# Performance work log

Measured on AMD Instinct MI355X. Metric: run time of the kernel, lower is better.

## Reference

```python
import jax, jax.numpy as jnp
import numpy as np

CUTOFF = 0.32178
SCALE = 2.0 * 28.0 * CUTOFF


def setup_inputs() -> dict:
    rng = np.random.default_rng(0)
    N, E0, K = 20000, 160000, 9
    pos_np = rng.uniform(0.0, 28.0, (N, 2)).astype(np.float32)
    s = rng.integers(0, N, E0)
    d = rng.integers(0, N, E0)
    keep = s != d
    ei = np.stack([s[keep], d[keep]])
    ei = np.concatenate([ei, ei[::-1]], axis=1)
    ei = np.unique(ei.T, axis=0).T.astype(np.int64)  # symmetric, deduped, no self-loops

    def ncut(ei_, pos_):
        r, c = ei_
        w = np.linalg.norm(pos_[r] - pos_[c], axis=1)
        deg = np.bincount(r, minlength=pos_.shape[0]).astype(np.float64)
        deg[deg == 0] = 1.0
        return w * (1.0 / deg[r] + 1.0 / deg[c])

    def graclus(ei_, w, n):
        # greedy heavy-weight matching in node-index order (graclus-style)
        o = np.argsort(ei_[0], kind='stable')
        r, c, ww = ei_[0][o], ei_[1][o], w[o]
        ptr = np.searchsorted(r, np.arange(n + 1))
        cl = -np.ones(n, dtype=np.int64)
        cid = 0
        for i in range(n):
            if cl[i] >= 0:
                continue
            best, bw = -1, -1.0
            for k in range(ptr[i], ptr[i + 1]):
                j = c[k]
                if cl[j] < 0 and j != i and ww[k] > bw:
                    bw, best = ww[k], j
            cl[i] = cid
            if best >= 0:
                cl[best] = cid
            cid += 1
        return cl, cid

    def pool_edges(ei_, cl):
        m = cl[ei_]
        m = m[:, m[0] != m[1]]
        return np.unique(m.T, axis=0).T

    def seg_mean(v, cl, c):
        out = np.zeros((c, v.shape[1]), dtype=np.float64)
        np.add.at(out, cl, v)
        cnt = np.bincount(cl, minlength=c).astype(np.float64)
        return (out / cnt[:, None]).astype(np.float32)

    cl1, C1 = graclus(ei, ncut(ei, pos_np), N)
    ei2 = pool_edges(ei, cl1)
    pos2 = seg_mean(pos_np, cl1, C1)
    cl2, C2 = graclus(ei2, ncut(ei2, pos2), C1)
    ei3 = pool_edges(ei2, cl2)

    def prm(*shape):
        return jnp.asarray(rng.normal(0.0, 0.1, shape).astype(np.float32))

    def sig(k):
        return jnp.asarray(rng.uniform(0.5, 1.5, (k, 2)).astype(np.float32))

    return {
        'x': jnp.asarray(rng.standard_normal((N, 1)).astype(np.float32)),
        'pos': jnp.asarray(pos_np),
        'edge_index1': jnp.asarray(ei, dtype=jnp.int32),
        'cluster1': jnp.asarray(cl1, dtype=jnp.int32),
        'edge_index2': jnp.asarray(ei2, dtype=jnp.int32),
        'cluster2': jnp.asarray(cl2, dtype=jnp.int32),
        'edge_index3': jnp.asarray(ei3, dtype=jnp.int32),
        'batch': jnp.zeros((C2,), dtype=jnp.int32),
        'g1': prm(1, K, 32), 'mu1': prm(K, 2) + 0.5, 'sigma1': sig(K), 'root1': prm(1, 32), 'b1': prm(32),
        'g2': prm(32, K, 64), 'mu2': prm(K, 2) + 0.5, 'sigma2': sig(K), 'root2': prm(32, 64), 'b2': prm(64),
        'g3': prm(64, K, 64), 'mu3': prm(K, 2) + 0.5, 'sigma3': sig(K), 'root3': prm(64, 64), 'b3': prm(64),
        'fw': prm(64, 128), 'fb': prm(128),
    }


def _pseudo(pos, ei):
    # edge pseudo-coordinates: (pos[col]-pos[row]) / (2*28*cutoff) + 0.5
    return (pos[ei[1]] - pos[ei[0]]) / SCALE + 0.5


def _gmm_conv(x, ei, ea, g, mu, sigma, root, bias, n):
    # GMMConv: mean over neighbors of sum_k gauss_k(e_ij) * (x_j @ G_k), plus root weight and bias
    row, col = ei[0], ei[1]
    d = ea[:, None, :] - mu[None]                                       # [E,K,2]
    w = jnp.exp(-0.5 * jnp.sum(d * d / (sigma[None] ** 2), axis=-1))    # [E,K]
    msg = jnp.einsum('ei,iko,ek->eo', x[row], g, w)                     # [E,out]
    agg = jax.ops.segment_sum(msg, col, num_segments=n)
    cnt = jax.ops.segment_sum(jnp.ones_like(col, dtype=x.dtype), col, num_segments=n)
    return agg / jnp.maximum(cnt, 1.0)[:, None] + x @ root + bias


def _seg_mean(v, seg, n):
    s = jax.ops.segment_sum(v, seg, num_segments=n)
    c = jax.ops.segment_sum(jnp.ones((v.shape[0],), v.dtype), seg, num_segments=n)
    return s / jnp.maximum(c, 1.0)[:, None]


def _forward(x, pos, edge_index1, cluster1, edge_index2, cluster2, edge_index3, batch,
             g1, mu1, sigma1, root1, b1, g2, mu2, sigma2, root2, b2,
             g3, mu3, sigma3, root3, b3, fw, fb):
    N = x.shape[0]
    C1 = cluster2.shape[0]
    C2 = batch.shape[0]
    h = jax.nn.elu(_gmm_conv(x, edge_index1, _pseudo(pos, edge_index1), g1, mu1, sigma1, root1, b1, N))
    h = jax.ops.segment_max(h, cluster1, num_segments=C1)               # max_pool x
    pos2 = _seg_mean(pos, cluster1, C1)                                  # max_pool pos (mean)
    h = jax.nn.elu(_gmm_conv(h, edge_index2, _pseudo(pos2, edge_index2), g2, mu2, sigma2, root2, b2, C1))
    h = jax.ops.segment_max(h, cluster2, num_segments=C2)
    pos3 = _seg_mean(pos2, cluster2, C2)
    h = jax.nn.elu(_gmm_conv(h, edge_index3, _pseudo(pos3, edge_index3), g3, mu3, sigma3, root3, b3, C2))
    gm = _seg_mean(h, batch, 1)                                          # global_mean_pool (1 graph)
    return gm @ fw + fb                                                  # forward returns fc1(x)


def reference(x, pos, edge_index1, cluster1, edge_index2, cluster2, edge_index3, batch,
              g1, mu1, sigma1, root1, b1, g2, mu2, sigma2, root2, b2,
              g3, mu3, sigma3, root3, b3, fw, fb):
    return _forward(x, pos, edge_index1, cluster1, edge_index2, cluster2, edge_index3, batch,
                    g1, mu1, sigma1, root1, b1, g2, mu2, sigma2, root2, b2,
                    g3, mu3, sigma3, root3, b3, fw, fb)
```

## Files before the change

### kernel.cpp

```cpp
#include <hip/hip_runtime.h>
#include <math.h>

static constexpr float SCALE_F = (float)(2.0 * 28.0 * 0.32178);

__device__ __forceinline__ unsigned mapf(float f){
    unsigned u = __float_as_uint(f);
    return (u & 0x80000000u) ? ~u : (u | 0x80000000u);
}
__device__ __forceinline__ float unmapf(unsigned m){
    unsigned u = (m & 0x80000000u) ? (m ^ 0x80000000u) : ~m;
    return __uint_as_float(u);
}
__device__ __forceinline__ float eluf(float x){ return x > 0.f ? x : expm1f(x); }

__device__ __forceinline__ void wave_sync(){
    __builtin_amdgcn_wave_barrier();
    asm volatile("s_waitcnt lgkmcnt(0)" ::: "memory");
    __builtin_amdgcn_wave_barrier();
}

__global__ void prep_kernel(const float* __restrict__ x, const float* __restrict__ pos, int N,
    const int* __restrict__ ei1, int E1, const int* __restrict__ ei2, int E2, int C1,
    const int* __restrict__ ei3, int E3, int C2,
    int* __restrict__ rp1, int* __restrict__ rp2, int* __restrict__ rp3,
    unsigned* __restrict__ hmax, int nmax, float* __restrict__ zreg, int nz,
    float4* __restrict__ xp1)
{
    int i0 = blockIdx.x*blockDim.x + threadIdx.x, gs = gridDim.x*blockDim.x;
    for (int i = i0; i < nmax; i += gs) hmax[i] = 0x007FFFFFu;
    for (int i = i0; i < nz;   i += gs) zreg[i] = 0.f;
    for (int i = i0; i < N;    i += gs) xp1[i] = make_float4(pos[2*i], pos[2*i+1], x[i], 0.f);
    int nrp = N + C1 + C2 + 3;
    for (int i = i0; i < nrp; i += gs){
        const int* rows; int E, n; int* rp;
        if (i <= N)            { rows = ei1; E = E1; n = i;            rp = rp1 + n; }
        else if (i <= N+1+C1)  { rows = ei2; E = E2; n = i - (N+1);    rp = rp2 + n; }
        else                   { rows = ei3; E = E3; n = i - (N+C1+2); rp = rp3 + n; }
        int lo = 0, hi = E;
        while (lo < hi){ int m = (lo+hi) >> 1; if (rows[m] < n) lo = m+1; else hi = m; }
        *rp = lo;
    }
}

__global__ __launch_bounds__(256) void l1_kernel(const float4* __restrict__ xp1,
    const int* __restrict__ ei1, int E1, const int* __restrict__ rp1, const int* __restrict__ cl1,
    const float* __restrict__ g1, const float* __restrict__ mu1, const float* __restrict__ sg1,
    const float* __restrict__ rt1, const float* __restrict__ b1,
    unsigned* __restrict__ h2m, float4* __restrict__ pos2s4, int N)
{
    int t = threadIdx.x;
    int lane = t & 63, wv = t >> 6;
    int q = lane >> 4, il = lane & 15;
    int n = (blockIdx.x*4 + wv)*4 + q;
    if (n >= N) return;
    const int* cols = ei1 + E1;
    float mx[9], my[9], ivx[9], ivy[9];
    #pragma unroll
    for (int k = 0; k < 9; k++){
        mx[k] = mu1[2*k]; my[k] = mu1[2*k+1];
        float sx = sg1[2*k], sy = sg1[2*k+1];
        ivx[k] = 1.f/(sx*sx); ivy[k] = 1.f/(sy*sy);
    }
    float4 me = xp1[n];
    float px = me.x, py = me.y, xn = me.z;
    int e0 = rp1[n], e1 = rp1[n+1];
    float s[9] = {0.f,0.f,0.f,0.f,0.f,0.f,0.f,0.f,0.f};
    for (int e = e0 + il; e < e1; e += 16){
        int j = cols[e];
        float4 pj = xp1[j];
        float ux = (px - pj.x)/SCALE_F + 0.5f;
        float uy = (py - pj.y)/SCALE_F + 0.5f;
        #pragma unroll
        for (int k = 0; k < 9; k++){
            float dx = ux - mx[k], dy = uy - my[k];
            s[k] += pj.z * expf(-0.5f*(dx*dx*ivx[k] + dy*dy*ivy[k]));
        }
    }
    #pragma unroll
    for (int off = 8; off > 0; off >>= 1){
        #pragma unroll
        for (int k = 0; k < 9; k++) s[k] += __shfl_xor(s[k], off, 16);
    }
    float inv = 1.f / (float)max(e1 - e0, 1);
    int c = cl1[n];
    #pragma unroll
    for (int oo = 0; oo < 2; oo++){
        int o = il + oo*16;
        float acc = 0.f;
        #pragma unroll
        for (int k = 0; k < 9; k++) acc += g1[k*32+o] * s[k];
        float v = acc*inv + xn*rt1[o] + b1[o];
        atomicMax(&h2m[(size_t)c*32 + o], mapf(eluf(v)));
    }
    if (il == 0){
        atomicAdd(&pos2s4[c].x, px);
        atomicAdd(&pos2s4[c].y, py);
        atomicAdd(&pos2s4[c].z, 1.f);
    }
}

__global__ __launch_bounds__(256) void l2_kernel(const unsigned* __restrict__ h2m,
    const float4* __restrict__ pos2s4,
    const int* __restrict__ ei2, int E2, const int* __restrict__ rp2, const int* __restrict__ cl2,
    const float* __restrict__ g2, const float* __restrict__ mu2, const float* __restrict__ sg2,
    const float* __restrict__ rt2, const float* __restrict__ b2,
    unsigned* __restrict__ h3m, float4* __restrict__ pos3s4, int C1)
{
    __shared__ float wbuf[4][576];
    __shared__ int   jcs[4][64];
    __shared__ float xns[4][32];
    int t = threadIdx.x, l = t & 63, w = t >> 6;
    int n = blockIdx.x*4 + w;
    if (n >= C1) return;
    const int* cols = ei2 + E2;
    float mx[9], my[9], ivx[9], ivy[9];
    #pragma unroll
    for (int k = 0; k < 9; k++){
        mx[k] = mu2[2*k]; my[k] = mu2[2*k+1];
        float sx = sg2[2*k], sy = sg2[2*k+1];
        ivx[k] = 1.f/(sx*sx); ivy[k] = 1.f/(sy*sy);
    }
    if (l < 32) xns[w][l] = unmapf(h2m[(size_t)n*32 + l]);
    float4 pm = pos2s4[n];
    float cn = fmaxf(pm.z, 1.f);
    float px = pm.x/cn, py = pm.y/cn;
    int e0 = rp2[n], e1 = rp2[n+1], deg = e1 - e0;
    int i = l & 31, half = l >> 5;
    float sacc[9] = {0.f,0.f,0.f,0.f,0.f,0.f,0.f,0.f,0.f};
    for (int base = e0; base < e1; base += 64){
        int ne = min(64, e1 - base);
        if (l < ne){
            int j = cols[base + l];
            jcs[w][l] = j;
            float4 pj = pos2s4[j];
            float cj = fmaxf(pj.z, 1.f);
            float ux = (px - pj.x/cj)/SCALE_F + 0.5f;
            float uy = (py - pj.y/cj)/SCALE_F + 0.5f;
            #pragma unroll
            for (int k = 0; k < 9; k++){
                float dx = ux - mx[k], dy = uy - my[k];
                wbuf[w][l*9+k] = expf(-0.5f*(dx*dx*ivx[k] + dy*dy*ivy[k]));
            }
        }
        wave_sync();
        for (int jj = half; jj < ne; jj += 2){
            int j = jcs[w][jj];
            float xji = unmapf(h2m[(size_t)j*32 + i]);
            #pragma unroll
            for (int k = 0; k < 9; k++) sacc[k] += xji * wbuf[w][jj*9+k];
        }
        wave_sync();
    }
    #pragma unroll
    for (int k = 0; k < 9; k++) sacc[k] += __shfl_xor(sacc[k], 32, 64);
    if (l < 32){
        #pragma unroll
        for (int k = 0; k < 9; k++) wbuf[w][l*9+k] = sacc[k];
    }
    wave_sync();
    float acc = 0.f;
    #pragma unroll 8
    for (int idx = 0; idx < 288; idx++) acc += g2[idx*64 + l] * wbuf[w][idx];
    float racc = 0.f;
    #pragma unroll 8
    for (int ii = 0; ii < 32; ii++) racc += xns[w][ii] * rt2[ii*64 + l];
    float inv = 1.f / (float)max(deg, 1);
    float h = eluf(acc*inv + racc + b2[l]);
    int c = cl2[n];
    atomicMax(&h3m[(size_t)c*64 + l], mapf(h));
    if (l == 0){
        atomicAdd(&pos3s4[c].x, px);
        atomicAdd(&pos3s4[c].y, py);
        atomicAdd(&pos3s4[c].z, 1.f);
    }
}

__global__ __launch_bounds__(256) void l3_kernel(const unsigned* __restrict__ h3m,
    const float4* __restrict__ pos3s4,
    const int* __restrict__ ei3, int E3, const int* __restrict__ rp3,
    const float* __restrict__ g3, const float* __restrict__ mu3, const float* __restrict__ sg3,
    const float* __restrict__ rt3, const float* __restrict__ b3,
    float* __restrict__ gpart, int C2)
{
    __shared__ float wbuf[4][576];
    __shared__ int   jcs[4][64];
    __shared__ float xns[4][64];
    int t = threadIdx.x, l = t & 63, w = t >> 6;
    int n = blockIdx.x*4 + w;
    if (n >= C2) return;
    const int* cols = ei3 + E3;
    float mx[9], my[9], ivx[9], ivy[9];
    #pragma unroll
    for (int k = 0; k < 9; k++){
        mx[k] = mu3[2*k]; my[k] = mu3[2*k+1];
        float sx = sg3[2*k], sy = sg3[2*k+1];
        ivx[k] = 1.f/(sx*sx); ivy[k] = 1.f/(sy*sy);
    }
    xns[w][l] = unmapf(h3m[(size_t)n*64 + l]);
    float4 pm = pos3s4[n];
    float cn = fmaxf(pm.z, 1.f);
    float px = pm.x/cn, py = pm.y/cn;
    int e0 = rp3[n], e1 = rp3[n+1], deg = e1 - e0;
    float sacc[9] = {0.f,0.f,0.f,0.f,0.f,0.f,0.f,0.f,0.f};
    for (int base = e0; base < e1; base += 64){
        int ne = min(64, e1 - base);
        if (l < ne){
            int j = cols[base + l];
            jcs[w][l] = j;
            float4 pj = pos3s4[j];
            float cj = fmaxf(pj.z, 1.f);
            float ux = (px - pj.x/cj)/SCALE_F + 0.5f;
            float uy = (py - pj.y/cj)/SCALE_F + 0.5f;
            #pragma unroll
            for (int k = 0; k < 9; k++){
                float dx = ux - mx[k], dy = uy - my[k];
                wbuf[w][l*9+k] = expf(-0.5f*(dx*dx*ivx[k] + dy*dy*ivy[k]));
            }
        }
        wave_sync();
        for (int jj = 0; jj < ne; jj++){
            int j = jcs[w][jj];
            float xji = unmapf(h3m[(size_t)j*64 + l]);
            #pragma unroll
            for (int k = 0; k < 9; k++) sacc[k] += xji * wbuf[w][jj*9+k];
        }
        wave_sync();
    }
    #pragma unroll
    for (int k = 0; k < 9; k++) wbuf[w][l*9+k] = sacc[k];
    wave_sync();
    float acc = 0.f;
    #pragma unroll 8
    for (int idx = 0; idx < 576; idx++) acc += g3[idx*64 + l] * wbuf[w][idx];
    float racc = 0.f;
    #pragma unroll 8
    for (int ii = 0; ii < 64; ii++) racc += xns[w][ii] * rt3[ii*64 + l];
    float inv = 1.f / (float)max(deg, 1);
    float h = eluf(acc*inv + racc + b3[l]);
    atomicAdd(&gpart[(size_t)(n & 63)*64 + l], h);
}

__global__ void final_kernel(const float* __restrict__ gpart, const float* __restrict__ fw,
                             const float* __restrict__ fb, float* __restrict__ out, int C2){
    __shared__ float gs[64];
    __shared__ float red[2*64];
    int t = threadIdx.x;
    int o = t & 63, h = t >> 6;
    float a = 0.f;
    for (int p = h*32; p < h*32 + 32; p++) a += gpart[p*64 + o];
    red[h*64 + o] = a;
    __syncthreads();
    if (t < 64) gs[t] = (red[t] + red[64+t]) / (float)C2;
    __syncthreads();
    float acc = fb[t];
    for (int o2 = 0; o2 < 64; o2++) acc += gs[o2] * fw[o2*128 + t];
    out[t] = acc;
}

extern "C" void kernel_launch(void* const* d_in, const int* in_sizes, int n_in,
                              void* d_out, int out_size, void* d_ws, size_t ws_size,
                              hipStream_t stream)
{
    const float* x    = (const float*)d_in[0];
    const float* pos  = (const float*)d_in[1];
    const int*   ei1  = (const int*)d_in[2];
    const int*   cl1  = (const int*)d_in[3];
    const int*   ei2  = (const int*)d_in[4];
    const int*   cl2  = (const int*)d_in[5];
    const int*   ei3  = (const int*)d_in[6];
    const float* g1   = (const float*)d_in[8];
    const float* mu1  = (const float*)d_in[9];
    const float* sg1  = (const float*)d_in[10];
    const float* rt1  = (const float*)d_in[11];
    const float* b1   = (const float*)d_in[12];
    const float* g2   = (const float*)d_in[13];
    const float* mu2  = (const float*)d_in[14];
    const float* sg2  = (const float*)d_in[15];
    const float* rt2  = (const float*)d_in[16];
    const float* b2   = (const float*)d_in[17];
    const float* g3   = (const float*)d_in[18];
    const float* mu3  = (const float*)d_in[19];
    const float* sg3  = (const float*)d_in[20];
    const float* rt3  = (const float*)d_in[21];
    const float* b3   = (const float*)d_in[22];
    const float* fw   = (const float*)d_in[23];
    const float* fb   = (const float*)d_in[24];
    float* out = (float*)d_out;

    const int N  = in_sizes[0];
    const int E1 = in_sizes[2] / 2;
    const int C1 = in_sizes[5];
    const int E2 = in_sizes[4] / 2;
    const int C2 = in_sizes[7];
    const int E3 = in_sizes[6] / 2;

    float* w = (float*)d_ws;
    size_t off = 0;
    float4* xp1    = (float4*)(w + off); off += (size_t)4*N;
    float4* pos2s4 = (float4*)(w + off); off += (size_t)4*C1;
    float4* pos3s4 = (float4*)(w + off); off += (size_t)4*C2;
    float*  gpart  = w + off;            off += 64*64;
    int* rp1 = (int*)(w + off); off += (size_t)N + 1;
    int* rp2 = (int*)(w + off); off += (size_t)C1 + 1;
    int* rp3 = (int*)(w + off); off += (size_t)C2 + 1;
    unsigned* h2m = (unsigned*)(w + off); off += (size_t)C1 * 32;
    unsigned* h3m = (unsigned*)(w + off); off += (size_t)C2 * 64;

    const int nmax = C1*32 + C2*64;
    const int nz   = 4*C1 + 4*C2 + 64*64;
    prep_kernel<<<dim3(1024), dim3(256), 0, stream>>>(x, pos, N,
        ei1, E1, ei2, E2, C1, ei3, E3, C2,
        rp1, rp2, rp3, h2m, nmax, (float*)pos2s4, nz, xp1);

    l1_kernel<<<dim3((N + 15)/16), dim3(256), 0, stream>>>(xp1, ei1, E1, rp1, cl1,
        g1, mu1, sg1, rt1, b1, h2m, pos2s4, N);
    l2_kernel<<<dim3((C1 + 3)/4), dim3(256), 0, stream>>>(h2m, pos2s4, ei2, E2, rp2, cl2,
        g2, mu2, sg2, rt2, b2, h3m, pos3s4, C1);
    l3_kernel<<<dim3((C2 + 3)/4), dim3(256), 0, stream>>>(h3m, pos3s4, ei3, E3, rp3,
        g3, mu3, sg3, rt3, b3, gpart, C2);
    final_kernel<<<dim3(1), dim3(128), 0, stream>>>(gpart, fw, fb, out, C2);
}
```

Baseline: 229.2 us.

## Replace atomic max/mean pooling with pair-gather pooling and split conv layers

Pooling no longer uses atomicMax into order-mapped integers or atomicAdd for centroids. A prep pass instead records the min and max node index of each cluster, and new pool kernels take the elementwise max and mean of those two members. Layers 2 and 3 are each split into an aggregation kernel, which writes per-node 9xC sums to a workspace buffer, and a dense projection kernel. Both use float4 LDS layouts and unrolled gather loops. This relies on every cluster having at most two members, which graclus matching guarantees. It adds several kernel launches and extra global round-trips for the intermediate sums.

```diff
diff --git a/kernel.cpp b/kernel.cpp
--- a/kernel.cpp
+++ b/kernel.cpp
@@ -3,14 +3,6 @@
 
 static constexpr float SCALE_F = (float)(2.0 * 28.0 * 0.32178);
 
-__device__ __forceinline__ unsigned mapf(float f){
-    unsigned u = __float_as_uint(f);
-    return (u & 0x80000000u) ? ~u : (u | 0x80000000u);
-}
-__device__ __forceinline__ float unmapf(unsigned m){
-    unsigned u = (m & 0x80000000u) ? (m ^ 0x80000000u) : ~m;
-    return __uint_as_float(u);
-}
 __device__ __forceinline__ float eluf(float x){ return x > 0.f ? x : expm1f(x); }
 
 __device__ __forceinline__ void wave_sync(){
@@ -19,17 +11,33 @@
     __builtin_amdgcn_wave_barrier();
 }
 
+__global__ void initk(int* __restrict__ mlo1, int* __restrict__ mhi1, int C1,
+                      int* __restrict__ mlo2, int* __restrict__ mhi2, int C2,
+                      float* __restrict__ gpart){
+    int i = blockIdx.x*blockDim.x + threadIdx.x, gs = gridDim.x*blockDim.x;
+    for (int c = i; c < C1; c += gs){ mlo1[c] = 0x7FFFFFFF; mhi1[c] = -1; }
+    for (int c = i; c < C2; c += gs){ mlo2[c] = 0x7FFFFFFF; mhi2[c] = -1; }
+    for (int k = i; k < 64*64; k += gs) gpart[k] = 0.f;
+}
+
 __global__ void prep_kernel(const float* __restrict__ x, const float* __restrict__ pos, int N,
     const int* __restrict__ ei1, int E1, const int* __restrict__ ei2, int E2, int C1,
     const int* __restrict__ ei3, int E3, int C2,
+    const int* __restrict__ cl1, const int* __restrict__ cl2,
     int* __restrict__ rp1, int* __restrict__ rp2, int* __restrict__ rp3,
-    unsigned* __restrict__ hmax, int nmax, float* __restrict__ zreg, int nz,
+    int* __restrict__ mlo1, int* __restrict__ mhi1, int* __restrict__ mlo2, int* __restrict__ mhi2,
     float4* __restrict__ xp1)
 {
     int i0 = blockIdx.x*blockDim.x + threadIdx.x, gs = gridDim.x*blockDim.x;
-    for (int i = i0; i < nmax; i += gs) hmax[i] = 0x007FFFFFu;
-    for (int i = i0; i < nz;   i += gs) zreg[i] = 0.f;
-    for (int i = i0; i < N;    i += gs) xp1[i] = make_float4(pos[2*i], pos[2*i+1], x[i], 0.f);
+    for (int i = i0; i < N; i += gs){
+        xp1[i] = make_float4(pos[2*i], pos[2*i+1], x[i], 0.f);
+        int c = cl1[i];
+        atomicMin(&mlo1[c], i); atomicMax(&mhi1[c], i);
+    }
+    for (int i = i0; i < C1; i += gs){
+        int c = cl2[i];
+        atomicMin(&mlo2[c], i); atomicMax(&mhi2[c], i);
+    }
     int nrp = N + C1 + C2 + 3;
     for (int i = i0; i < nrp; i += gs){
         const int* rows; int E, n; int* rp;
@@ -43,10 +51,10 @@
 }
 
 __global__ __launch_bounds__(256) void l1_kernel(const float4* __restrict__ xp1,
-    const int* __restrict__ ei1, int E1, const int* __restrict__ rp1, const int* __restrict__ cl1,
+    const int* __restrict__ ei1, int E1, const int* __restrict__ rp1,
     const float* __restrict__ g1, const float* __restrict__ mu1, const float* __restrict__ sg1,
     const float* __restrict__ rt1, const float* __restrict__ b1,
-    unsigned* __restrict__ h2m, float4* __restrict__ pos2s4, int N)
+    float* __restrict__ h1, int N)
 {
     int t = threadIdx.x;
     int lane = t & 63, wv = t >> 6;
@@ -82,33 +90,43 @@
         for (int k = 0; k < 9; k++) s[k] += __shfl_xor(s[k], off, 16);
     }
     float inv = 1.f / (float)max(e1 - e0, 1);
-    int c = cl1[n];
     #pragma unroll
     for (int oo = 0; oo < 2; oo++){
         int o = il + oo*16;
         float acc = 0.f;
         #pragma unroll
         for (int k = 0; k < 9; k++) acc += g1[k*32+o] * s[k];
-        float v = acc*inv + xn*rt1[o] + b1[o];
-        atomicMax(&h2m[(size_t)c*32 + o], mapf(eluf(v)));
-    }
-    if (il == 0){
-        atomicAdd(&pos2s4[c].x, px);
-        atomicAdd(&pos2s4[c].y, py);
-        atomicAdd(&pos2s4[c].z, 1.f);
-    }
-}
-
-__global__ __launch_bounds__(256) void l2_kernel(const unsigned* __restrict__ h2m,
+        h1[(size_t)n*32 + o] = eluf(acc*inv + xn*rt1[o] + b1[o]);
+    }
+}
+
+__global__ void pool1_kernel(const float* __restrict__ h1, const float4* __restrict__ xp1,
+    const int* __restrict__ mlo1, const int* __restrict__ mhi1,
+    float* __restrict__ h2, float4* __restrict__ pos2s4, int C1)
+{
+    int i0 = blockIdx.x*blockDim.x + threadIdx.x, gs = gridDim.x*blockDim.x;
+    for (int idx = i0; idx < C1*32; idx += gs){
+        int c = idx >> 5, i = idx & 31;
+        h2[idx] = fmaxf(h1[(size_t)mlo1[c]*32 + i], h1[(size_t)mhi1[c]*32 + i]);
+    }
+    for (int c = i0; c < C1; c += gs){
+        int a = mlo1[c], b = mhi1[c];
+        float4 pa = xp1[a];
+        float px, py;
+        if (a == b){ px = pa.x; py = pa.y; }
+        else { float4 pb = xp1[b]; px = (pa.x + pb.x)/2.f; py = (pa.y + pb.y)/2.f; }
+        pos2s4[c] = make_float4(px, py, 0.f, 0.f);
+    }
+}
+
+__global__ __launch_bounds__(256) void l2a_kernel(const float* __restrict__ h2,
     const float4* __restrict__ pos2s4,
-    const int* __restrict__ ei2, int E2, const int* __restrict__ rp2, const int* __restrict__ cl2,
-    const float* __restrict__ g2, const float* __restrict__ mu2, const float* __restrict__ sg2,
-    const float* __restrict__ rt2, const float* __restrict__ b2,
-    unsigned* __restrict__ h3m, float4* __restrict__ pos3s4, int C1)
-{
-    __shared__ float wbuf[4][576];
-    __shared__ int   jcs[4][64];
-    __shared__ float xns[4][32];
+    const int* __restrict__ ei2, int E2, const int* __restrict__ rp2,
+    const float* __restrict__ mu2, const float* __restrict__ sg2,
+    float* __restrict__ S2, int C1)
+{
+    __shared__ __align__(16) float wbuf[4][768];
+    __shared__ int jcs[4][64];
     int t = threadIdx.x, l = t & 63, w = t >> 6;
     int n = blockIdx.x*4 + w;
     if (n >= C1) return;
@@ -120,11 +138,9 @@
         float sx = sg2[2*k], sy = sg2[2*k+1];
         ivx[k] = 1.f/(sx*sx); ivy[k] = 1.f/(sy*sy);
     }
-    if (l < 32) xns[w][l] = unmapf(h2m[(size_t)n*32 + l]);
     float4 pm = pos2s4[n];
-    float cn = fmaxf(pm.z, 1.f);
-    float px = pm.x/cn, py = pm.y/cn;
-    int e0 = rp2[n], e1 = rp2[n+1], deg = e1 - e0;
+    float px = pm.x, py = pm.y;
+    int e0 = rp2[n], e1 = rp2[n+1];
     int i = l & 31, half = l >> 5;
     float sacc[9] = {0.f,0.f,0.f,0.f,0.f,0.f,0.f,0.f,0.f};
     for (int base = e0; base < e1; base += 64){
@@ -133,21 +149,48 @@
             int j = cols[base + l];
             jcs[w][l] = j;
             float4 pj = pos2s4[j];
-            float cj = fmaxf(pj.z, 1.f);
-            float ux = (px - pj.x/cj)/SCALE_F + 0.5f;
-            float uy = (py - pj.y/cj)/SCALE_F + 0.5f;
+            float ux = (px - pj.x)/SCALE_F + 0.5f;
+            float uy = (py - pj.y)/SCALE_F + 0.5f;
+            float wk[9];
             #pragma unroll
             for (int k = 0; k < 9; k++){
                 float dx = ux - mx[k], dy = uy - my[k];
-                wbuf[w][l*9+k] = expf(-0.5f*(dx*dx*ivx[k] + dy*dy*ivy[k]));
+                wk[k] = expf(-0.5f*(dx*dx*ivx[k] + dy*dy*ivy[k]));
             }
+            *(float4*)&wbuf[w][l*12]     = make_float4(wk[0], wk[1], wk[2], wk[3]);
+            *(float4*)&wbuf[w][l*12 + 4] = make_float4(wk[4], wk[5], wk[6], wk[7]);
+            wbuf[w][l*12 + 8] = wk[8];
         }
         wave_sync();
-        for (int jj = half; jj < ne; jj += 2){
+        int jj = half;
+        for (; jj + 6 < ne; jj += 8){
+            int j0 = jcs[w][jj],   j1 = jcs[w][jj+2];
+            int j2 = jcs[w][jj+4], j3 = jcs[w][jj+6];
+            float x0 = h2[(size_t)j0*32 + i];
+            float x1 = h2[(size_t)j1*32 + i];
+            float x2 = h2[(size_t)j2*32 + i];
+            float x3 = h2[(size_t)j3*32 + i];
+            #pragma unroll
+            for (int u = 0; u < 4; u++){
+                int jc = jj + 2*u;
+                float xv = (u==0)?x0:(u==1)?x1:(u==2)?x2:x3;
+                float4 wa = *(const float4*)&wbuf[w][jc*12];
+                float4 wb = *(const float4*)&wbuf[w][jc*12 + 4];
+                float  w8 = wbuf[w][jc*12 + 8];
+                sacc[0] += xv*wa.x; sacc[1] += xv*wa.y; sacc[2] += xv*wa.z; sacc[3] += xv*wa.w;
+                sacc[4] += xv*wb.x; sacc[5] += xv*wb.y; sacc[6] += xv*wb.z; sacc[7] += xv*wb.w;
+                sacc[8] += xv*w8;
+            }
+        }
+        for (; jj < ne; jj += 2){
             int j = jcs[w][jj];
-            float xji = unmapf(h2m[(size_t)j*32 + i]);
-            #pragma unroll
-            for (int k = 0; k < 9; k++) sacc[k] += xji * wbuf[w][jj*9+k];
+            float xv = h2[(size_t)j*32 + i];
+            float4 wa = *(const float4*)&wbuf[w][jj*12];
+            float4 wb = *(const float4*)&wbuf[w][jj*12 + 4];
+            float  w8 = wbuf[w][jj*12 + 8];
+            sacc[0] += xv*wa.x; sacc[1] += xv*wa.y; sacc[2] += xv*wa.z; sacc[3] += xv*wa.w;
+            sacc[4] += xv*wb.x; sacc[5] += xv*wb.y; sacc[6] += xv*wb.z; sacc[7] += xv*wb.w;
+            sacc[8] += xv*w8;
         }
         wave_sync();
     }
@@ -155,36 +198,83 @@
     for (int k = 0; k < 9; k++) sacc[k] += __shfl_xor(sacc[k], 32, 64);
     if (l < 32){
         #pragma unroll
-        for (int k = 0; k < 9; k++) wbuf[w][l*9+k] = sacc[k];
-    }
+        for (int k = 0; k < 9; k++) S2[(size_t)n*288 + l*9 + k] = sacc[k];
+    }
+}
+
+__global__ __launch_bounds__(256) void l2b_kernel(const float* __restrict__ S2,
+    const float* __restrict__ h2, const int* __restrict__ rp2,
+    const float* __restrict__ g2, const float* __restrict__ rt2, const float* __restrict__ b2,
+    float* __restrict__ h2out, int C1)
+{
+    __shared__ __align__(16) float sbuf[4][288];
+    __shared__ __align__(16) float xns[4][32];
+    int t = threadIdx.x, l = t & 63, w = t >> 6;
+    int n = blockIdx.x*4 + w;
+    if (n >= C1) return;
+    const float4* srow = (const float4*)(S2 + (size_t)n*288);
+    *(float4*)&sbuf[w][l*4] = srow[l];
+    if (l < 8) *(float4*)&sbuf[w][(64+l)*4] = srow[64+l];
+    if (l < 32) xns[w][l] = h2[(size_t)n*32 + l];
     wave_sync();
+    const float* gcol = g2 + l;
     float acc = 0.f;
-    #pragma unroll 8
-    for (int idx = 0; idx < 288; idx++) acc += g2[idx*64 + l] * wbuf[w][idx];
+    #pragma unroll 4
+    for (int qq = 0; qq < 36; qq++){
+        int ib = qq*8;
+        float g0 = gcol[(ib+0)*64], g1v = gcol[(ib+1)*64];
+        float g2v = gcol[(ib+2)*64], g3 = gcol[(ib+3)*64];
+        float g4 = gcol[(ib+4)*64], g5 = gcol[(ib+5)*64];
+        float g6 = gcol[(ib+6)*64], g7 = gcol[(ib+7)*64];
+        float4 sa = *(const float4*)&sbuf[w][ib];
+        float4 sb = *(const float4*)&sbuf[w][ib+4];
+        acc += g0*sa.x; acc += g1v*sa.y; acc += g2v*sa.z; acc += g3*sa.w;
+        acc += g4*sb.x; acc += g5*sb.y; acc += g6*sb.z; acc += g7*sb.w;
+    }
+    const float* rcol = rt2 + l;
     float racc = 0.f;
-    #pragma unroll 8
-    for (int ii = 0; ii < 32; ii++) racc += xns[w][ii] * rt2[ii*64 + l];
+    #pragma unroll 2
+    for (int qq = 0; qq < 4; qq++){
+        int ib = qq*8;
+        float4 xa = *(const float4*)&xns[w][ib];
+        float4 xb = *(const float4*)&xns[w][ib+4];
+        racc += rcol[(ib+0)*64]*xa.x; racc += rcol[(ib+1)*64]*xa.y;
+        racc += rcol[(ib+2)*64]*xa.z; racc += rcol[(ib+3)*64]*xa.w;
+        racc += rcol[(ib+4)*64]*xb.x; racc += rcol[(ib+5)*64]*xb.y;
+        racc += rcol[(ib+6)*64]*xb.z; racc += rcol[(ib+7)*64]*xb.w;
+    }
+    int deg = rp2[n+1] - rp2[n];
     float inv = 1.f / (float)max(deg, 1);
-    float h = eluf(acc*inv + racc + b2[l]);
-    int c = cl2[n];
-    atomicMax(&h3m[(size_t)c*64 + l], mapf(h));
-    if (l == 0){
-        atomicAdd(&pos3s4[c].x, px);
-        atomicAdd(&pos3s4[c].y, py);
-        atomicAdd(&pos3s4[c].z, 1.f);
-    }
-}
-
-__global__ __launch_bounds__(256) void l3_kernel(const unsigned* __restrict__ h3m,
+    h2out[(size_t)n*64 + l] = eluf(acc*inv + racc + b2[l]);
+}
+
+__global__ void pool2_kernel(const float* __restrict__ h2out, const float4* __restrict__ pos2s4,
+    const int* __restrict__ mlo2, const int* __restrict__ mhi2,
+    float* __restrict__ h3, float4* __restrict__ pos3s4, int C2)
+{
+    int i0 = blockIdx.x*blockDim.x + threadIdx.x, gs = gridDim.x*blockDim.x;
+    for (int idx = i0; idx < C2*64; idx += gs){
+        int c = idx >> 6, i = idx & 63;
+        h3[idx] = fmaxf(h2out[(size_t)mlo2[c]*64 + i], h2out[(size_t)mhi2[c]*64 + i]);
+    }
+    for (int c = i0; c < C2; c += gs){
+        int a = mlo2[c], b = mhi2[c];
+        float4 pa = pos2s4[a];
+        float px, py;
+        if (a == b){ px = pa.x; py = pa.y; }
+        else { float4 pb = pos2s4[b]; px = (pa.x + pb.x)/2.f; py = (pa.y + pb.y)/2.f; }
+        pos3s4[c] = make_float4(px, py, 0.f, 0.f);
+    }
+}
+
+__global__ __launch_bounds__(256) void l3a_kernel(const float* __restrict__ h3,
     const float4* __restrict__ pos3s4,
     const int* __restrict__ ei3, int E3, const int* __restrict__ rp3,
-    const float* __restrict__ g3, const float* __restrict__ mu3, const float* __restrict__ sg3,
-    const float* __restrict__ rt3, const float* __restrict__ b3,
-    float* __restrict__ gpart, int C2)
-{
-    __shared__ float wbuf[4][576];
-    __shared__ int   jcs[4][64];
-    __shared__ float xns[4][64];
+    const float* __restrict__ mu3, const float* __restrict__ sg3,
+    float* __restrict__ S3, int C2)
+{
+    __shared__ __align__(16) float wbuf[4][768];
+    __shared__ int jcs[4][64];
     int t = threadIdx.x, l = t & 63, w = t >> 6;
     int n = blockIdx.x*4 + w;
     if (n >= C2) return;
@@ -196,11 +286,9 @@
         float sx = sg3[2*k], sy = sg3[2*k+1];
         ivx[k] = 1.f/(sx*sx); ivy[k] = 1.f/(sy*sy);
     }
-    xns[w][l] = unmapf(h3m[(size_t)n*64 + l]);
     float4 pm = pos3s4[n];
-    float cn = fmaxf(pm.z, 1.f);
-    float px = pm.x/cn, py = pm.y/cn;
-    int e0 = rp3[n], e1 = rp3[n+1], deg = e1 - e0;
+    float px = pm.x, py = pm.y;
+    int e0 = rp3[n], e1 = rp3[n+1];
     float sacc[9] = {0.f,0.f,0.f,0.f,0.f,0.f,0.f,0.f,0.f};
     for (int base = e0; base < e1; base += 64){
         int ne = min(64, e1 - base);
@@ -208,33 +296,98 @@
             int j = cols[base + l];
             jcs[w][l] = j;
             float4 pj = pos3s4[j];
-            float cj = fmaxf(pj.z, 1.f);
-            float ux = (px - pj.x/cj)/SCALE_F + 0.5f;
-            float uy = (py - pj.y/cj)/SCALE_F + 0.5f;
+            float ux = (px - pj.x)/SCALE_F + 0.5f;
+            float uy = (py - pj.y)/SCALE_F + 0.5f;
+            float wk[9];
             #pragma unroll
             for (int k = 0; k < 9; k++){
                 float dx = ux - mx[k], dy = uy - my[k];
-                wbuf[w][l*9+k] = expf(-0.5f*(dx*dx*ivx[k] + dy*dy*ivy[k]));
+                wk[k] = expf(-0.5f*(dx*dx*ivx[k] + dy*dy*ivy[k]));
             }
+            *(float4*)&wbuf[w][l*12]     = make_float4(wk[0], wk[1], wk[2], wk[3]);
+            *(float4*)&wbuf[w][l*12 + 4] = make_float4(wk[4], wk[5], wk[6], wk[7]);
+            wbuf[w][l*12 + 8] = wk[8];
         }
         wave_sync();
-        for (int jj = 0; jj < ne; jj++){
+        int jj = 0;
+        for (; jj + 3 < ne; jj += 4){
+            int j0 = jcs[w][jj],   j1 = jcs[w][jj+1];
+            int j2 = jcs[w][jj+2], j3 = jcs[w][jj+3];
+            float x0 = h3[(size_t)j0*64 + l];
+            float x1 = h3[(size_t)j1*64 + l];
+            float x2 = h3[(size_t)j2*64 + l];
+            float x3 = h3[(size_t)j3*64 + l];
+            #pragma unroll
+            for (int u = 0; u < 4; u++){
+                int jc = jj + u;
+                float xv = (u==0)?x0:(u==1)?x1:(u==2)?x2:x3;
+                float4 wa = *(const float4*)&wbuf[w][jc*12];
+                float4 wb = *(const float4*)&wbuf[w][jc*12 + 4];
+                float  w8 = wbuf[w][jc*12 + 8];
+                sacc[0] += xv*wa.x; sacc[1] += xv*wa.y; sacc[2] += xv*wa.z; sacc[3] += xv*wa.w;
+                sacc[4] += xv*wb.x; sacc[5] += xv*wb.y; sacc[6] += xv*wb.z; sacc[7] += xv*wb.w;
+                sacc[8] += xv*w8;
+            }
+        }
+        for (; jj < ne; jj++){
             int j = jcs[w][jj];
-            float xji = unmapf(h3m[(size_t)j*64 + l]);
-            #pragma unroll
-            for (int k = 0; k < 9; k++) sacc[k] += xji * wbuf[w][jj*9+k];
+            float xv = h3[(size_t)j*64 + l];
+            float4 wa = *(const float4*)&wbuf[w][jj*12];
+            float4 wb = *(const float4*)&wbuf[w][jj*12 + 4];
+            float  w8 = wbuf[w][jj*12 + 8];
+            sacc[0] += xv*wa.x; sacc[1] += xv*wa.y; sacc[2] += xv*wa.z; sacc[3] += xv*wa.w;
+            sacc[4] += xv*wb.x; sacc[5] += xv*wb.y; sacc[6] += xv*wb.z; sacc[7] += xv*wb.w;
+            sacc[8] += xv*w8;
         }
         wave_sync();
     }
     #pragma unroll
-    for (int k = 0; k < 9; k++) wbuf[w][l*9+k] = sacc[k];
+    for (int k = 0; k < 9; k++) S3[(size_t)n*576 + l*9 + k] = sacc[k];
+}
+
+__global__ __launch_bounds__(256) void l3b_kernel(const float* __restrict__ S3,
+    const float* __restrict__ h3, const int* __restrict__ rp3,
+    const float* __restrict__ g3, const float* __restrict__ rt3, const float* __restrict__ b3,
+    float* __restrict__ gpart, int C2)
+{
+    __shared__ __align__(16) float sbuf[4][576];
+    __shared__ __align__(16) float xns[4][64];
+    int t = threadIdx.x, l = t & 63, w = t >> 6;
+    int n = blockIdx.x*4 + w;
+    if (n >= C2) return;
+    const float4* srow = (const float4*)(S3 + (size_t)n*576);
+    *(float4*)&sbuf[w][l*4] = srow[l];
+    *(float4*)&sbuf[w][(64+l)*4] = srow[64+l];
+    if (l < 16) *(float4*)&sbuf[w][(128+l)*4] = srow[128+l];
+    xns[w][l] = h3[(size_t)n*64 + l];
     wave_sync();
+    const float* gcol = g3 + l;
     float acc = 0.f;
-    #pragma unroll 8
-    for (int idx = 0; idx < 576; idx++) acc += g3[idx*64 + l] * wbuf[w][idx];
+    #pragma unroll 4
+    for (int qq = 0; qq < 72; qq++){
+        int ib = qq*8;
+        float g0 = gcol[(ib+0)*64], g1v = gcol[(ib+1)*64];
+        float g2v = gcol[(ib+2)*64], g3v = gcol[(ib+3)*64];
+        float g4 = gcol[(ib+4)*64], g5 = gcol[(ib+5)*64];
+        float g6 = gcol[(ib+6)*64], g7 = gcol[(ib+7)*64];
+        float4 sa = *(const float4*)&sbuf[w][ib];
+        float4 sb = *(const float4*)&sbuf[w][ib+4];
+        acc += g0*sa.x; acc += g1v*sa.y; acc += g2v*sa.z; acc += g3v*sa.w;
+        acc += g4*sb.x; acc += g5*sb.y; acc += g6*sb.z; acc += g7*sb.w;
+    }
+    const float* rcol = rt3 + l;
     float racc = 0.f;
-    #pragma unroll 8
-    for (int ii = 0; ii < 64; ii++) racc += xns[w][ii] * rt3[ii*64 + l];
+    #pragma unroll 2
+    for (int qq = 0; qq < 8; qq++){
+        int ib = qq*8;
+        float4 xa = *(const float4*)&xns[w][ib];
+        float4 xb = *(const float4*)&xns[w][ib+4];
+        racc += rcol[(ib+0)*64]*xa.x; racc += rcol[(ib+1)*64]*xa.y;
+        racc += rcol[(ib+2)*64]*xa.z; racc += rcol[(ib+3)*64]*xa.w;
+        racc += rcol[(ib+4)*64]*xb.x; racc += rcol[(ib+5)*64]*xb.y;
+        racc += rcol[(ib+6)*64]*xb.z; racc += rcol[(ib+7)*64]*xb.w;
+    }
+    int deg = rp3[n+1] - rp3[n];
     float inv = 1.f / (float)max(deg, 1);
     float h = eluf(acc*inv + racc + b3[l]);
     atomicAdd(&gpart[(size_t)(n & 63)*64 + l], h);
@@ -299,24 +452,36 @@
     float4* xp1    = (float4*)(w + off); off += (size_t)4*N;
     float4* pos2s4 = (float4*)(w + off); off += (size_t)4*C1;
     float4* pos3s4 = (float4*)(w + off); off += (size_t)4*C2;
-    float*  gpart  = w + off;            off += 64*64;
-    int* rp1 = (int*)(w + off); off += (size_t)N + 1;
-    int* rp2 = (int*)(w + off); off += (size_t)C1 + 1;
-    int* rp3 = (int*)(w + off); off += (size_t)C2 + 1;
-    unsigned* h2m = (unsigned*)(w + off); off += (size_t)C1 * 32;
-    unsigned* h3m = (unsigned*)(w + off); off += (size_t)C2 * 64;
-
-    const int nmax = C1*32 + C2*64;
-    const int nz   = 4*C1 + 4*C2 + 64*64;
-    prep_kernel<<<dim3(1024), dim3(256), 0, stream>>>(x, pos, N,
-        ei1, E1, ei2, E2, C1, ei3, E3, C2,
-        rp1, rp2, rp3, h2m, nmax, (float*)pos2s4, nz, xp1);
-
-    l1_kernel<<<dim3((N + 15)/16), dim3(256), 0, stream>>>(xp1, ei1, E1, rp1, cl1,
-        g1, mu1, sg1, rt1, b1, h2m, pos2s4, N);
-    l2_kernel<<<dim3((C1 + 3)/4), dim3(256), 0, stream>>>(h2m, pos2s4, ei2, E2, rp2, cl2,
-        g2, mu2, sg2, rt2, b2, h3m, pos3s4, C1);
-    l3_kernel<<<dim3((C2 + 3)/4), dim3(256), 0, stream>>>(h3m, pos3s4, ei3, E3, rp3,
-        g3, mu3, sg3, rt3, b3, gpart, C2);
+    size_t sbig = (size_t)288*C1 > (size_t)576*C2 ? (size_t)288*C1 : (size_t)576*C2;
+    float* Sbig = w + off; off += sbig;
+    float* h1    = w + off; off += (size_t)32*N;
+    float* h2    = w + off; off += (size_t)32*C1;
+    float* h2out = w + off; off += (size_t)64*C1;
+    float* h3    = w + off; off += (size_t)64*C2;
+    float* gpart = w + off; off += 64*64;
+    int* rp1  = (int*)(w + off); off += (size_t)N + 1;
+    int* rp2  = (int*)(w + off); off += (size_t)C1 + 1;
+    int* rp3  = (int*)(w + off); off += (size_t)C2 + 1;
+    int* mlo1 = (int*)(w + off); off += (size_t)C1;
+    int* mhi1 = (int*)(w + off); off += (size_t)C1;
+    int* mlo2 = (int*)(w + off); off += (size_t)C2;
+    int* mhi2 = (int*)(w + off); off += (size_t)C2;
+
+    initk<<<dim3(64), dim3(256), 0, stream>>>(mlo1, mhi1, C1, mlo2, mhi2, C2, gpart);
+    prep_kernel<<<dim3(512), dim3(256), 0, stream>>>(x, pos, N,
+        ei1, E1, ei2, E2, C1, ei3, E3, C2, cl1, cl2,
+        rp1, rp2, rp3, mlo1, mhi1, mlo2, mhi2, xp1);
+    l1_kernel<<<dim3((N + 15)/16), dim3(256), 0, stream>>>(xp1, ei1, E1, rp1,
+        g1, mu1, sg1, rt1, b1, h1, N);
+    pool1_kernel<<<dim3(1024), dim3(256), 0, stream>>>(h1, xp1, mlo1, mhi1, h2, pos2s4, C1);
+    l2a_kernel<<<dim3((C1 + 3)/4), dim3(256), 0, stream>>>(h2, pos2s4, ei2, E2, rp2,
+        mu2, sg2, Sbig, C1);
+    l2b_kernel<<<dim3((C1 + 3)/4), dim3(256), 0, stream>>>(Sbig, h2, rp2,
+        g2, rt2, b2, h2out, C1);
+    pool2_kernel<<<dim3(512), dim3(256), 0, stream>>>(h2out, pos2s4, mlo2, mhi2, h3, pos3s4, C2);
+    l3a_kernel<<<dim3((C2 + 3)/4), dim3(256), 0, stream>>>(h3, pos3s4, ei3, E3, rp3,
+        mu3, sg3, Sbig, C2);
+    l3b_kernel<<<dim3((C2 + 3)/4), dim3(256), 0, stream>>>(Sbig, h3, rp3,
+        g3, rt3, b3, gpart, C2);
     final_kernel<<<dim3(1), dim3(128), 0, stream>>>(gpart, fw, fb, out, C2);
 }
```

Measured after the change: 236.2 us. 3.1% more time.
